# Optimization experiments

Measured on AMD Instinct MI355X. Metric: run time of the kernel, lower is better.

## Reference

```python
import jax, jax.numpy as jnp
import numpy as np

N = 131072
F_DIM = 128
HID = 256
POL = 512
EPS = 1e-5


def _lin(key, fan_in, fan_out):
    k1, k2 = jax.random.split(key)
    s = 1.0 / np.sqrt(fan_in)
    W = jax.random.uniform(k1, (fan_in, fan_out), jnp.float32, -s, s)
    b = jax.random.uniform(k2, (fan_out,), jnp.float32, -s, s)
    return W, b


def setup_inputs() -> dict:
    key = jax.random.key(0)
    ks = jax.random.split(key, 12)
    observation = jax.random.normal(ks[0], (N, F_DIM), jnp.float32)
    mask = jnp.ones((N, 1), jnp.float32)
    # dense_to_sparse(eye(N)) -> pure self-loop edge list
    ar = jnp.arange(N, dtype=jnp.int32)
    edge_index = jnp.stack([ar, ar])  # [2, N]
    W1, b1 = _lin(ks[1], F_DIM, HID)
    Wg, bg = _lin(ks[2], HID, HID)     # GCNConv weight/bias
    ln_w = jnp.ones((HID,), jnp.float32)
    ln_b = jnp.zeros((HID,), jnp.float32)
    Wgate, bgate = _lin(ks[3], HID, 1)
    Wd, bd = _lin(ks[4], HID, HID)
    Wp1, bp1 = _lin(ks[5], HID, POL)
    Wp2, bp2 = _lin(ks[6], POL, POL)
    Wv, bv = _lin(ks[7], POL, 1)
    return dict(observation=observation, mask=mask, edge_index=edge_index,
                W1=W1, b1=b1, Wg=Wg, bg=bg, ln_w=ln_w, ln_b=ln_b,
                Wgate=Wgate, bgate=bgate, Wd=Wd, bd=bd,
                Wp1=Wp1, bp1=bp1, Wp2=Wp2, bp2=bp2, Wv=Wv, bv=bv)


def reference(observation, mask, edge_index, W1, b1, Wg, bg, ln_w, ln_b,
              Wgate, bgate, Wd, bd, Wp1, bp1, Wp2, bp2, Wv, bv):
    n = observation.shape[0]
    # encoder_1 + relu
    X = jax.nn.relu(observation @ W1 + b1)  # [N,256]

    # GCNConv(256,256): add self-loops, symmetric norm, gather/scatter
    ar = jnp.arange(n, dtype=edge_index.dtype)
    ei = jnp.concatenate([edge_index, jnp.stack([ar, ar])], axis=1)  # [2,E+N]
    row, col = ei[0], ei[1]
    Xw = X @ Wg
    deg = jax.ops.segment_sum(jnp.ones(ei.shape[1], X.dtype), col, num_segments=n)
    dinv = jnp.where(deg > 0, jax.lax.rsqrt(deg), 0.0)
    norm = dinv[row] * dinv[col]
    msg = Xw[row] * norm[:, None]
    Xg = jax.ops.segment_sum(msg, col, num_segments=n) + bg
    Xg = jax.nn.relu(Xg)

    # PyG LayerNorm, mode='graph' (batch=None): global mean/std over all elements
    mu = Xg.mean()
    sd = jnp.sqrt(jnp.mean((Xg - mu) ** 2))  # std, unbiased=False
    Xn = (Xg - mu) / (sd + EPS) * ln_w + ln_b

    # AttentionalAggregation with sigmoid gate -> [1,256]
    gate = jax.nn.sigmoid(Xn @ Wgate + bgate)  # [N,1]
    pooled = jnp.sum(gate * Xn, axis=0, keepdims=True)

    h = jax.nn.relu(pooled @ Wd + bd)
    h = jax.nn.relu(h @ Wp1 + bp1)
    h = jax.nn.relu(h @ Wp2 + bp2)
    value = h @ Wv + bv  # [1,1]
    return value * mask  # broadcast -> [N,1]
```

## Files before the change

### kernel.cpp

```cpp
#include <hip/hip_runtime.h>

#define NROWS 131072
#define EPSV 1e-5f

typedef __attribute__((ext_vector_type(8))) short short8;
typedef __attribute__((ext_vector_type(4))) float floatx4;

__device__ __forceinline__ short f2bf(float f){
  unsigned u = __builtin_bit_cast(unsigned, f);
  u = (u + 0x7FFFu + ((u >> 16) & 1u)) >> 16;
  return (short)u;
}
__device__ __forceinline__ float bf2f(unsigned h){
  unsigned u = h << 16;
  return __builtin_bit_cast(float, u);
}

__device__ __forceinline__ int XIDX(int row, int col){
  return row*256 + ((((col >> 3) ^ (row & 31))) << 3) + (col & 7);
}

__global__ __launch_bounds__(256) void prep_kernel(
    const float* __restrict__ W1, const float* __restrict__ Wg,
    const float* __restrict__ lnw, const float* __restrict__ lnb,
    const float* __restrict__ Wgate,
    short* __restrict__ W1s, short* __restrict__ Wgs,
    float* __restrict__ u, float* accum)
{
  const int b = blockIdx.x, tid = threadIdx.x;
  if (b < 16){
    int idx = b*256 + tid;
    int lane = idx & 63, rg = idx >> 6;
    int ctg = rg & 15, kt = rg >> 4;
    int kb = kt*32 + (lane>>4)*8;
    int c  = ctg*16 + (lane&15);
    short8 t;
    #pragma unroll
    for (int j=0;j<8;j++) t[j] = f2bf(W1[(kb+j)*256 + c]);
    *(short8*)(W1s + idx*8) = t;
  } else if (b < 48){
    int idx = (b-16)*256 + tid;
    int lane = idx & 63, rg = idx >> 6;
    int ctg = rg & 15, kt = rg >> 4;
    int kb = kt*32 + (lane>>4)*8;
    int c  = ctg*16 + (lane&15);
    short8 t;
    #pragma unroll
    for (int j=0;j<8;j++) t[j] = f2bf(Wg[(kb+j)*256 + c]);
    *(short8*)(Wgs + idx*8) = t;
  } else {
    __shared__ float red[8];
    float uv = lnw[tid] * Wgate[tid];
    float lv = lnb[tid] * Wgate[tid];
    u[tid] = uv;
    float a = uv, c = lv;
    #pragma unroll
    for (int off=32; off; off >>= 1){
      a += __shfl_down(a, off);
      c += __shfl_down(c, off);
    }
    const int w = tid >> 6, l = tid & 63;
    if (l == 0){ red[w] = a; red[4+w] = c; }
    __syncthreads();
    if (tid == 0){
      accum[4] = red[0]+red[1]+red[2]+red[3];
      accum[5] = red[4]+red[5]+red[6]+red[7];
    }
  }
}

__global__ __launch_bounds__(256, 3) void gemm12_kernel(
    const float* __restrict__ obs, const float* __restrict__ b1,
    const float* __restrict__ bg,
    const short* __restrict__ W1s, const short* __restrict__ Wgs,
    const float* __restrict__ u,
    short* __restrict__ Xg, float* __restrict__ d, float* __restrict__ pS)
{
  __shared__ short Xs[64*256];
  __shared__ float dacc[64*33];
  short* As = Xs;
  const int tid = threadIdx.x;
  const int w = tid >> 6, l = tid & 63, q = l >> 4, lm = l & 15;
  const long R = (long)blockIdx.x * 64;

  short8 bc[4], bn[4];
  #pragma unroll
  for (int ct=0; ct<4; ct++)
    bc[ct] = *(const short8*)(W1s + (((w*4+ct))*64 + l)*8);

  #pragma unroll
  for (int rt=0; rt<4; rt++){
    const float* ap = obs + (R + rt*16 + lm)*128 + w*32 + q*8;
    floatx4 f0 = *(const floatx4*)ap;
    floatx4 f1 = *(const floatx4*)(ap + 4);
    short8 t;
    t[0]=f2bf(f0[0]); t[1]=f2bf(f0[1]); t[2]=f2bf(f0[2]); t[3]=f2bf(f0[3]);
    t[4]=f2bf(f1[0]); t[5]=f2bf(f1[1]); t[6]=f2bf(f1[2]); t[7]=f2bf(f1[3]);
    *(short8*)(As + ((w*4 + rt)*64 + l)*8) = t;
  }
  __syncthreads();

  floatx4 acc[4][4];
  #pragma unroll
  for (int a=0;a<4;a++)
    #pragma unroll
    for (int c=0;c<4;c++) acc[a][c] = (floatx4){0.f,0.f,0.f,0.f};

  short8 ac[4], an[4];
  #pragma unroll
  for (int rt=0; rt<4; rt++)
    ac[rt] = *(const short8*)(As + ((0*4 + rt)*64 + l)*8);
  #pragma unroll
  for (int kt=0; kt<4; kt++){
    if (kt < 3){
      #pragma unroll
      for (int ct=0; ct<4; ct++)
        bn[ct] = *(const short8*)(W1s + (((kt+1)*16 + (w*4+ct))*64 + l)*8);
      #pragma unroll
      for (int rt=0; rt<4; rt++)
        an[rt] = *(const short8*)(As + (((kt+1)*4 + rt)*64 + l)*8);
    }
    #pragma unroll
    for (int ct=0; ct<4; ct++)
      #pragma unroll
      for (int rt=0; rt<4; rt++)
        acc[rt][ct] = __builtin_amdgcn_mfma_f32_16x16x32_bf16(ac[rt], bc[ct], acc[rt][ct], 0,0,0);
    if (kt < 3){
      #pragma unroll
      for (int i=0;i<4;i++){ bc[i]=bn[i]; ac[i]=an[i]; }
    }
  }

  #pragma unroll
  for (int ct=0; ct<4; ct++)
    bc[ct] = *(const short8*)(Wgs + (((w*4+ct))*64 + l)*8);

  __syncthreads();

  #pragma unroll
  for (int ct=0; ct<4; ct++){
    const int col = w*64 + ct*16 + lm;
    const float bias = b1[col];
    #pragma unroll
    for (int rt=0; rt<4; rt++)
      #pragma unroll
      for (int r=0;r<4;r++){
        float v = acc[rt][ct][r] + bias;
        v = v > 0.f ? v : 0.f;
        Xs[XIDX(rt*16 + q*4 + r, col)] = f2bf(v);
      }
  }
  __syncthreads();

  #pragma unroll
  for (int a=0;a<4;a++)
    #pragma unroll
    for (int c=0;c<4;c++) acc[a][c] = (floatx4){0.f,0.f,0.f,0.f};

  #pragma unroll
  for (int rt=0; rt<4; rt++)
    ac[rt] = *(const short8*)(Xs + XIDX(rt*16 + lm, 0*32 + q*8));
  #pragma unroll
  for (int kt=0; kt<8; kt++){
    if (kt < 7){
      #pragma unroll
      for (int ct=0; ct<4; ct++)
        bn[ct] = *(const short8*)(Wgs + (((kt+1)*16 + (w*4+ct))*64 + l)*8);
      #pragma unroll
      for (int rt=0; rt<4; rt++)
        an[rt] = *(const short8*)(Xs + XIDX(rt*16 + lm, (kt+1)*32 + q*8));
    }
    #pragma unroll
    for (int ct=0; ct<4; ct++)
      #pragma unroll
      for (int rt=0; rt<4; rt++)
        acc[rt][ct] = __builtin_amdgcn_mfma_f32_16x16x32_bf16(ac[rt], bc[ct], acc[rt][ct], 0,0,0);
    if (kt < 7){
      #pragma unroll
      for (int i=0;i<4;i++){ bc[i]=bn[i]; ac[i]=an[i]; }
    }
  }
  __syncthreads();

  float s1 = 0.f, s2 = 0.f;
  #pragma unroll
  for (int ct=0; ct<4; ct++){
    const int col = w*64 + ct*16 + lm;
    const float bias = bg[col];
    #pragma unroll
    for (int rt=0; rt<4; rt++)
      #pragma unroll
      for (int r=0;r<4;r++){
        float v = acc[rt][ct][r] + bias;
        v = v > 0.f ? v : 0.f;
        s1 += v; s2 += v*v;
        Xs[XIDX(rt*16 + q*4 + r, col)] = f2bf(v);
      }
  }
  __syncthreads();

  const int cs = tid & 31;
  floatx4 u0 = *(const floatx4*)(u + cs*8);
  floatx4 u1 = *(const floatx4*)(u + cs*8 + 4);
  #pragma unroll
  for (int i=0;i<8;i++){
    int f = tid + 256*i;
    int row = f >> 5;
    short8 v = *(const short8*)(Xs + row*256 + ((cs ^ (row & 31)) << 3));
    *(short8*)(Xg + (R + row)*256 + cs*8) = v;
    float dp = bf2f((unsigned short)v[0])*u0[0] + bf2f((unsigned short)v[1])*u0[1]
             + bf2f((unsigned short)v[2])*u0[2] + bf2f((unsigned short)v[3])*u0[3]
             + bf2f((unsigned short)v[4])*u1[0] + bf2f((unsigned short)v[5])*u1[1]
             + bf2f((unsigned short)v[6])*u1[2] + bf2f((unsigned short)v[7])*u1[3];
    dacc[row*33 + cs] = dp;
  }

  #pragma unroll
  for (int off=32; off; off >>= 1){
    s1 += __shfl_down(s1, off);
    s2 += __shfl_down(s2, off);
  }
  if (l == 0){
    pS[blockIdx.x*4 + w] = s1;
    pS[8192 + blockIdx.x*4 + w] = s2;
  }
  __syncthreads();

  {
    const int row = tid >> 2, part = tid & 3;
    const float* dr = dacc + row*33 + part*8;
    float s = ((dr[0]+dr[1])+(dr[2]+dr[3])) + ((dr[4]+dr[5])+(dr[6]+dr[7]));
    s += __shfl_xor(s, 1);
    s += __shfl_xor(s, 2);
    if (part == 0) d[R + row] = s;
  }
}

__global__ __launch_bounds__(256) void stats_kernel(
    const float* __restrict__ pS, float* accum)
{
  __shared__ float red[8];
  const int tid = threadIdx.x, w = tid >> 6, l = tid & 63;
  float a = 0.f, b = 0.f;
  #pragma unroll
  for (int i=0;i<32;i++){
    a += pS[tid + 256*i];
    b += pS[8192 + tid + 256*i];
  }
  #pragma unroll
  for (int off=32; off; off >>= 1){
    a += __shfl_down(a, off);
    b += __shfl_down(b, off);
  }
  if (l == 0){ red[w] = a; red[4+w] = b; }
  __syncthreads();
  if (tid == 0){
    accum[0] = red[0]+red[1]+red[2]+red[3];
    accum[1] = red[4]+red[5]+red[6]+red[7];
  }
}

__global__ __launch_bounds__(256) void gatepool_kernel(
    const unsigned short* __restrict__ Xg, const float* __restrict__ d,
    const float* __restrict__ lnw, const float* __restrict__ lnb,
    const float* __restrict__ bgate, const float* __restrict__ accum,
    float* __restrict__ partials)
{
  __shared__ float sp[8][256];
  const int tid = threadIdx.x, w = tid >> 6, l = tid & 63;
  const int ro = l >> 5, c0 = (l & 31) * 8;
  const float NE = (float)NROWS * 256.f;
  const float mu = accum[0] / NE;
  float var = accum[1] / NE - mu*mu;
  var = var > 0.f ? var : 0.f;
  const float inv = 1.f / (sqrtf(var) + EPSV);
  const float gc = -inv*mu*accum[4] + accum[5] + bgate[0];
  float A[8], B[8];
  #pragma unroll
  for (int j=0;j<8;j++){
    float lw = lnw[c0+j];
    A[j] = inv*lw;
    B[j] = lnb[c0+j] - mu*inv*lw;
  }
  float p[8];
  #pragma unroll
  for (int j=0;j<8;j++) p[j] = 0.f;

  int row = blockIdx.x*8 + w*2 + ro;
  for (int it=0; it<16; it++, row += 8192){
    const float gate = 1.f / (1.f + __expf(-(inv*d[row] + gc)));
    short8 xv = *(const short8*)(Xg + (long)row*256 + c0);
    #pragma unroll
    for (int j=0;j<8;j++)
      p[j] += gate * (bf2f((unsigned short)xv[j])*A[j] + B[j]);
  }
  #pragma unroll
  for (int j=0;j<8;j++) sp[w*2+ro][c0+j] = p[j];
  __syncthreads();
  float s = sp[0][tid]+sp[1][tid]+sp[2][tid]+sp[3][tid]
          + sp[4][tid]+sp[5][tid]+sp[6][tid]+sp[7][tid];
  partials[tid*1024 + blockIdx.x] = s;
}

__global__ __launch_bounds__(256) void pool_reduce(
    const float* __restrict__ partials, float* accum)
{
  __shared__ float red[4];
  const int c = blockIdx.x, tid = threadIdx.x, w = tid >> 6, l = tid & 63;
  const float* p = partials + c*1024;
  float s = p[tid] + p[tid+256] + p[tid+512] + p[tid+768];
  #pragma unroll
  for (int off=32; off; off >>= 1) s += __shfl_down(s, off);
  if (l == 0) red[w] = s;
  __syncthreads();
  if (tid == 0) accum[8 + c] = red[0]+red[1]+red[2]+red[3];
}

__global__ __launch_bounds__(256) void mlp_wide(
    const float* __restrict__ W, const float* __restrict__ bias,
    const float* __restrict__ x, float* __restrict__ y,
    const int inDim, const int outDim, const int doRelu)
{
  __shared__ float sp[4][64];
  const int l = threadIdx.x & 63, w = threadIdx.x >> 6;
  const int j = blockIdx.x*64 + l;
  const int kq = inDim >> 2, k0 = w*kq;
  const float* wp = W + (long)k0*outDim + j;
  float p0=0.f,p1=0.f,p2=0.f,p3=0.f;
  for (int k=0; k<kq; k+=4){
    p0 += x[k0+k  ] * wp[(long)(k  )*outDim];
    p1 += x[k0+k+1] * wp[(long)(k+1)*outDim];
    p2 += x[k0+k+2] * wp[(long)(k+2)*outDim];
    p3 += x[k0+k+3] * wp[(long)(k+3)*outDim];
  }
  sp[w][l] = (p0+p1)+(p2+p3);
  __syncthreads();
  if (w == 0){
    float v = sp[0][l]+sp[1][l]+sp[2][l]+sp[3][l] + bias[j];
    if (doRelu) v = v > 0.f ? v : 0.f;
    y[j] = v;
  }
}

__global__ __launch_bounds__(64) void mlp_dot(
    const float* __restrict__ Wv, const float* __restrict__ bv,
    const float* __restrict__ x, float* __restrict__ y)
{
  const int l = threadIdx.x;
  float p = 0.f;
  for (int k = l; k < 512; k += 64) p += x[k]*Wv[k];
  #pragma unroll
  for (int off=1; off<64; off<<=1) p += __shfl_xor(p, off);
  if (l == 0) y[0] = p + bv[0];
}

__global__ __launch_bounds__(256) void bcast_kernel(
    const float* __restrict__ mask, const float* __restrict__ accum,
    float* __restrict__ out)
{
  const int i = blockIdx.x*256 + threadIdx.x;
  const float v = accum[2];
  floatx4 m = *(const floatx4*)(mask + (long)i*4);
  floatx4 o = {m[0]*v, m[1]*v, m[2]*v, m[3]*v};
  *(floatx4*)(out + (long)i*4) = o;
}

extern "C" void kernel_launch(void* const* d_in, const int* in_sizes, int n_in,
                              void* d_out, int out_size, void* d_ws, size_t ws_size,
                              hipStream_t stream)
{
  const float* obs   = (const float*)d_in[0];
  const float* mask  = (const float*)d_in[1];
  const float* W1    = (const float*)d_in[3];
  const float* b1    = (const float*)d_in[4];
  const float* Wg    = (const float*)d_in[5];
  const float* bg    = (const float*)d_in[6];
  const float* lnw   = (const float*)d_in[7];
  const float* lnb   = (const float*)d_in[8];
  const float* Wgate = (const float*)d_in[9];
  const float* bgate = (const float*)d_in[10];
  const float* Wd    = (const float*)d_in[11];
  const float* bd    = (const float*)d_in[12];
  const float* Wp1   = (const float*)d_in[13];
  const float* bp1   = (const float*)d_in[14];
  const float* Wp2   = (const float*)d_in[15];
  const float* bp2   = (const float*)d_in[16];
  const float* Wv    = (const float*)d_in[17];
  const float* bv    = (const float*)d_in[18];
  float* out = (float*)d_out;

  char* wsb = (char*)d_ws;
  short* Xg    = (short*)(wsb);
  short* W1s   = (short*)(wsb + 67108864);
  short* Wgs   = (short*)(wsb + 67174400);
  float* u     = (float*)(wsb + 67305472);
  float* dvec  = (float*)(wsb + 67306496);
  float* pS    = (float*)(wsb + 67830784);
  float* pPool = (float*)(wsb + 67896320);
  float* accum = (float*)(wsb + 68944896);

  prep_kernel<<<49, 256, 0, stream>>>(W1, Wg, lnw, lnb, Wgate, W1s, Wgs, u, accum);
  gemm12_kernel<<<2048, 256, 0, stream>>>(obs, b1, bg, W1s, Wgs, u, Xg, dvec, pS);
  stats_kernel<<<1, 256, 0, stream>>>(pS, accum);
  gatepool_kernel<<<1024, 256, 0, stream>>>((const unsigned short*)Xg, dvec,
                                            lnw, lnb, bgate, accum, pPool);
  pool_reduce<<<256, 256, 0, stream>>>(pPool, accum);
  mlp_wide<<<4, 256, 0, stream>>>(Wd,  bd,  accum+8,    accum+272,  256, 256, 1);
  mlp_wide<<<8, 256, 0, stream>>>(Wp1, bp1, accum+272,  accum+528,  256, 512, 1);
  mlp_wide<<<8, 256, 0, stream>>>(Wp2, bp2, accum+528,  accum+1040, 512, 512, 1);
  mlp_dot<<<1, 64, 0, stream>>>(Wv, bv, accum+1040, accum+2);
  bcast_kernel<<<128, 256, 0, stream>>>(mask, accum, out);
}
```

Baseline: 248.3 us.

## Fuse stats into gatepool and MLP chain with broadcast into one kernel

Removes the single-block stats kernel. gemm12 now reduces its partial sums per block, and each gatepool block re-reduces the 2048 per-block partials itself. The four tiny MLP kernels and the broadcast are merged into one kernel. Each of its 32 blocks recomputes the whole MLP redundantly and then writes its slice of the output. This cuts seven kernel launches down to three at the cost of redundant small work per block. It also switches the bf16 rounding to the cheaper round-half-up form and uses fmaxf for ReLU.

```diff
diff --git a/kernel.cpp b/kernel.cpp
--- a/kernel.cpp
+++ b/kernel.cpp
@@ -8,8 +8,7 @@
 
 __device__ __forceinline__ short f2bf(float f){
   unsigned u = __builtin_bit_cast(unsigned, f);
-  u = (u + 0x7FFFu + ((u >> 16) & 1u)) >> 16;
-  return (short)u;
+  return (short)((u + 0x8000u) >> 16);
 }
 __device__ __forceinline__ float bf2f(unsigned h){
   unsigned u = h << 16;
@@ -78,6 +77,7 @@
 {
   __shared__ short Xs[64*256];
   __shared__ float dacc[64*33];
+  __shared__ float sred[8];
   short* As = Xs;
   const int tid = threadIdx.x;
   const int w = tid >> 6, l = tid & 63, q = l >> 4, lm = l & 15;
@@ -145,8 +145,7 @@
     for (int rt=0; rt<4; rt++)
       #pragma unroll
       for (int r=0;r<4;r++){
-        float v = acc[rt][ct][r] + bias;
-        v = v > 0.f ? v : 0.f;
+        float v = fmaxf(acc[rt][ct][r] + bias, 0.f);
         Xs[XIDX(rt*16 + q*4 + r, col)] = f2bf(v);
       }
   }
@@ -191,8 +190,7 @@
     for (int rt=0; rt<4; rt++)
       #pragma unroll
       for (int r=0;r<4;r++){
-        float v = acc[rt][ct][r] + bias;
-        v = v > 0.f ? v : 0.f;
+        float v = fmaxf(acc[rt][ct][r] + bias, 0.f);
         s1 += v; s2 += v*v;
         Xs[XIDX(rt*16 + q*4 + r, col)] = f2bf(v);
       }
@@ -220,10 +218,7 @@
     s1 += __shfl_down(s1, off);
     s2 += __shfl_down(s2, off);
   }
-  if (l == 0){
-    pS[blockIdx.x*4 + w] = s1;
-    pS[8192 + blockIdx.x*4 + w] = s2;
-  }
+  if (l == 0){ sred[w] = s1; sred[4+w] = s2; }
   __syncthreads();
 
   {
@@ -234,46 +229,49 @@
     s += __shfl_xor(s, 2);
     if (part == 0) d[R + row] = s;
   }
-}
-
-__global__ __launch_bounds__(256) void stats_kernel(
-    const float* __restrict__ pS, float* accum)
-{
-  __shared__ float red[8];
-  const int tid = threadIdx.x, w = tid >> 6, l = tid & 63;
-  float a = 0.f, b = 0.f;
-  #pragma unroll
-  for (int i=0;i<32;i++){
-    a += pS[tid + 256*i];
-    b += pS[8192 + tid + 256*i];
-  }
-  #pragma unroll
-  for (int off=32; off; off >>= 1){
-    a += __shfl_down(a, off);
-    b += __shfl_down(b, off);
-  }
-  if (l == 0){ red[w] = a; red[4+w] = b; }
-  __syncthreads();
-  if (tid == 0){
-    accum[0] = red[0]+red[1]+red[2]+red[3];
-    accum[1] = red[4]+red[5]+red[6]+red[7];
-  }
+  if (tid == 0) pS[blockIdx.x]        = sred[0]+sred[1]+sred[2]+sred[3];
+  if (tid == 1) pS[2048 + blockIdx.x] = sred[4]+sred[5]+sred[6]+sred[7];
 }
 
 __global__ __launch_bounds__(256) void gatepool_kernel(
     const unsigned short* __restrict__ Xg, const float* __restrict__ d,
     const float* __restrict__ lnw, const float* __restrict__ lnb,
-    const float* __restrict__ bgate, const float* __restrict__ accum,
-    float* __restrict__ partials)
+    const float* __restrict__ bgate, const float* __restrict__ pS,
+    const float* __restrict__ accum, float* __restrict__ partials)
 {
   __shared__ float sp[8][256];
+  __shared__ float sred[8];
+  __shared__ float sMI[2];
   const int tid = threadIdx.x, w = tid >> 6, l = tid & 63;
   const int ro = l >> 5, c0 = (l & 31) * 8;
-  const float NE = (float)NROWS * 256.f;
-  const float mu = accum[0] / NE;
-  float var = accum[1] / NE - mu*mu;
-  var = var > 0.f ? var : 0.f;
-  const float inv = 1.f / (sqrtf(var) + EPSV);
+
+  {
+    float a = 0.f, b = 0.f;
+    #pragma unroll
+    for (int i=0;i<8;i++){
+      a += pS[tid + 256*i];
+      b += pS[2048 + tid + 256*i];
+    }
+    #pragma unroll
+    for (int off=32; off; off >>= 1){
+      a += __shfl_down(a, off);
+      b += __shfl_down(b, off);
+    }
+    if (l == 0){ sred[w] = a; sred[4+w] = b; }
+    __syncthreads();
+    if (tid == 0){
+      const float NE = (float)NROWS * 256.f;
+      float S1 = sred[0]+sred[1]+sred[2]+sred[3];
+      float S2 = sred[4]+sred[5]+sred[6]+sred[7];
+      float mu = S1 / NE;
+      float var = S2 / NE - mu*mu;
+      var = var > 0.f ? var : 0.f;
+      sMI[0] = mu;
+      sMI[1] = 1.f / (sqrtf(var) + EPSV);
+    }
+    __syncthreads();
+  }
+  const float mu = sMI[0], inv = sMI[1];
   const float gc = -inv*mu*accum[4] + accum[5] + bgate[0];
   float A[8], B[8];
   #pragma unroll
@@ -316,53 +314,68 @@
   if (tid == 0) accum[8 + c] = red[0]+red[1]+red[2]+red[3];
 }
 
-__global__ __launch_bounds__(256) void mlp_wide(
-    const float* __restrict__ W, const float* __restrict__ bias,
-    const float* __restrict__ x, float* __restrict__ y,
-    const int inDim, const int outDim, const int doRelu)
-{
-  __shared__ float sp[4][64];
-  const int l = threadIdx.x & 63, w = threadIdx.x >> 6;
-  const int j = blockIdx.x*64 + l;
-  const int kq = inDim >> 2, k0 = w*kq;
-  const float* wp = W + (long)k0*outDim + j;
-  float p0=0.f,p1=0.f,p2=0.f,p3=0.f;
-  for (int k=0; k<kq; k+=4){
-    p0 += x[k0+k  ] * wp[(long)(k  )*outDim];
-    p1 += x[k0+k+1] * wp[(long)(k+1)*outDim];
-    p2 += x[k0+k+2] * wp[(long)(k+2)*outDim];
-    p3 += x[k0+k+3] * wp[(long)(k+3)*outDim];
-  }
-  sp[w][l] = (p0+p1)+(p2+p3);
-  __syncthreads();
-  if (w == 0){
-    float v = sp[0][l]+sp[1][l]+sp[2][l]+sp[3][l] + bias[j];
-    if (doRelu) v = v > 0.f ? v : 0.f;
-    y[j] = v;
-  }
-}
-
-__global__ __launch_bounds__(64) void mlp_dot(
-    const float* __restrict__ Wv, const float* __restrict__ bv,
-    const float* __restrict__ x, float* __restrict__ y)
-{
-  const int l = threadIdx.x;
-  float p = 0.f;
-  for (int k = l; k < 512; k += 64) p += x[k]*Wv[k];
-  #pragma unroll
-  for (int off=1; off<64; off<<=1) p += __shfl_xor(p, off);
-  if (l == 0) y[0] = p + bv[0];
-}
-
-__global__ __launch_bounds__(256) void bcast_kernel(
-    const float* __restrict__ mask, const float* __restrict__ accum,
+__global__ __launch_bounds__(256) void mlp_bcast(
+    const float* __restrict__ Wd,  const float* __restrict__ bd,
+    const float* __restrict__ Wp1, const float* __restrict__ bp1,
+    const float* __restrict__ Wp2, const float* __restrict__ bp2,
+    const float* __restrict__ Wv,  const float* __restrict__ bv,
+    const float* __restrict__ accum, const float* __restrict__ mask,
     float* __restrict__ out)
 {
-  const int i = blockIdx.x*256 + threadIdx.x;
-  const float v = accum[2];
-  floatx4 m = *(const floatx4*)(mask + (long)i*4);
-  floatx4 o = {m[0]*v, m[1]*v, m[2]*v, m[3]*v};
-  *(floatx4*)(out + (long)i*4) = o;
+  __shared__ float xa[512], xb[512];
+  __shared__ float red[4];
+  const int tid = threadIdx.x, w = tid >> 6, l = tid & 63;
+
+  xa[tid] = accum[8 + tid];
+  __syncthreads();
+  {
+    float s = 0.f;
+    #pragma unroll 8
+    for (int k=0; k<256; k++) s += xa[k] * Wd[k*256 + tid];
+    xb[tid] = fmaxf(s + bd[tid], 0.f);
+  }
+  __syncthreads();
+  {
+    float s0 = 0.f, s1 = 0.f;
+    #pragma unroll 8
+    for (int k=0; k<256; k++){
+      float x = xb[k];
+      s0 += x * Wp1[k*512 + tid];
+      s1 += x * Wp1[k*512 + tid + 256];
+    }
+    xa[tid]       = fmaxf(s0 + bp1[tid], 0.f);
+    xa[tid + 256] = fmaxf(s1 + bp1[tid + 256], 0.f);
+  }
+  __syncthreads();
+  {
+    float s0 = 0.f, s1 = 0.f;
+    #pragma unroll 8
+    for (int k=0; k<512; k++){
+      float x = xa[k];
+      s0 += x * Wp2[k*512 + tid];
+      s1 += x * Wp2[k*512 + tid + 256];
+    }
+    xb[tid]       = fmaxf(s0 + bp2[tid], 0.f);
+    xb[tid + 256] = fmaxf(s1 + bp2[tid + 256], 0.f);
+  }
+  __syncthreads();
+  {
+    float p = xb[tid]*Wv[tid] + xb[tid+256]*Wv[tid+256];
+    #pragma unroll
+    for (int off=32; off; off >>= 1) p += __shfl_down(p, off);
+    if (l == 0) red[w] = p;
+  }
+  __syncthreads();
+  const float value = red[0]+red[1]+red[2]+red[3] + bv[0];
+
+  const long base = (long)blockIdx.x * 1024;
+  #pragma unroll
+  for (int i=0;i<4;i++){
+    long idx = base + i*256 + tid;
+    floatx4 m = *(const floatx4*)(mask + idx*4);
+    floatx4 o = {m[0]*value, m[1]*value, m[2]*value, m[3]*value};
+    *(floatx4*)(out + idx*4) = o;
+  }
 }
 
 extern "C" void kernel_launch(void* const* d_in, const int* in_sizes, int n_in,
@@ -396,18 +409,14 @@
   float* u     = (float*)(wsb + 67305472);
   float* dvec  = (float*)(wsb + 67306496);
   float* pS    = (float*)(wsb + 67830784);
-  float* pPool = (float*)(wsb + 67896320);
-  float* accum = (float*)(wsb + 68944896);
+  float* pPool = (float*)(wsb + 67847168);
+  float* accum = (float*)(wsb + 68895744);
 
   prep_kernel<<<49, 256, 0, stream>>>(W1, Wg, lnw, lnb, Wgate, W1s, Wgs, u, accum);
   gemm12_kernel<<<2048, 256, 0, stream>>>(obs, b1, bg, W1s, Wgs, u, Xg, dvec, pS);
-  stats_kernel<<<1, 256, 0, stream>>>(pS, accum);
   gatepool_kernel<<<1024, 256, 0, stream>>>((const unsigned short*)Xg, dvec,
-                                            lnw, lnb, bgate, accum, pPool);
+                                            lnw, lnb, bgate, pS, accum, pPool);
   pool_reduce<<<256, 256, 0, stream>>>(pPool, accum);
-  mlp_wide<<<4, 256, 0, stream>>>(Wd,  bd,  accum+8,    accum+272,  256, 256, 1);
-  mlp_wide<<<8, 256, 0, stream>>>(Wp1, bp1, accum+272,  accum+528,  256, 512, 1);
-  mlp_wide<<<8, 256, 0, stream>>>(Wp2, bp2, accum+528,  accum+1040, 512, 512, 1);
-  mlp_dot<<<1, 64, 0, stream>>>(Wv, bv, accum+1040, accum+2);
-  bcast_kernel<<<128, 256, 0, stream>>>(mask, accum, out);
-}
+  mlp_bcast<<<32, 256, 0, stream>>>(Wd, bd, Wp1, bp1, Wp2, bp2, Wv, bv,
+                                    accum, mask, out);
+}
```

After: 277.3 us. +11.7%, slower.
